# Performance work log

Measured on AMD Instinct MI355X. Metric: run time of the kernel, lower is better.

The kernel has to match this reference:

```python
import jax, jax.numpy as jnp
import numpy as np

TEMPERATURE = 0.07
N_CLASSES = 100


def setup_inputs() -> dict:
    key = jax.random.key(0)
    k1, k2 = jax.random.split(key)
    N, D = 8192, 128
    emb = jax.random.normal(k1, (N, D), dtype=jnp.float32)
    # unit-normalize so exp(sim / temperature) stays finite in fp32
    emb = emb / jnp.linalg.norm(emb, axis=1, keepdims=True)
    labels = jax.random.randint(k2, (N,), 0, N_CLASSES, dtype=jnp.int64)
    return {"embeddings": emb, "labels": labels}


def reference(embeddings, labels):
    N = embeddings.shape[0]
    dt = embeddings.dtype
    # [N, N] similarity
    sim = jnp.matmul(embeddings, embeddings.T) / TEMPERATURE
    off_diag = 1.0 - jnp.eye(N, dtype=dt)
    pos_mask = (labels[:, None] == labels[None, :]).astype(dt) * off_diag
    exp_sim = jnp.exp(sim) * off_diag  # diagonal zeroed
    positive_sum = jnp.sum(exp_sim * pos_mask, axis=1)
    total_sum = jnp.sum(exp_sim, axis=1)
    loss = -jnp.log(positive_sum / (total_sum + 1e-8) + 1e-8)
    valid = pos_mask.sum(axis=1) > 0
    cnt = jnp.sum(valid.astype(dt))
    mean_loss = jnp.where(
        cnt > 0,
        jnp.sum(jnp.where(valid, loss, jnp.zeros_like(loss))) / jnp.maximum(cnt, 1.0),
        jnp.asarray(0.0, dtype=dt),
    )
    return mean_loss
```

## Files before the change

### kernel.cpp

```cpp
#include <hip/hip_runtime.h>

#define N 8192
#define D 128
#define SCALE_A 20.6098592f
#define NBX 64
#define NBY 8
#define NBLK (NBX * NBY)

using short8  = __attribute__((ext_vector_type(8))) short;
using float4v = __attribute__((ext_vector_type(4))) float;

#if __has_builtin(__builtin_amdgcn_exp2f)
#define EXP2(x) __builtin_amdgcn_exp2f(x)
#else
#define EXP2(x) __expf((x) * 0.69314718f)
#endif

static __device__ inline unsigned int f2bf(float f) {
    union { float f; unsigned int u; } x;
    x.f = f;
    unsigned int u = x.u;
    return (u + 0x7FFFu + ((u >> 16) & 1u)) >> 16;
}

__global__ __launch_bounds__(256) void cl_prep(
    const float* __restrict__ emb, unsigned short* __restrict__ bfBf,
    unsigned short* __restrict__ bfAf, float* __restrict__ tot,
    int* __restrict__ ticket)
{
    const int t = blockIdx.x * 256 + threadIdx.x;
    const int row   = t >> 4;
    const int chunk = t & 15;
    const float* p = emb + (size_t)row * D + chunk * 8;
    float4v f0 = *(const float4v*)p;
    float4v f1 = *(const float4v*)(p + 4);
    uint4 ub, ua;
    ub.x = f2bf(f0[0]) | (f2bf(f0[1]) << 16);
    ub.y = f2bf(f0[2]) | (f2bf(f0[3]) << 16);
    ub.z = f2bf(f1[0]) | (f2bf(f1[1]) << 16);
    ub.w = f2bf(f1[2]) | (f2bf(f1[3]) << 16);
    ua.x = f2bf(f0[0] * SCALE_A) | (f2bf(f0[1] * SCALE_A) << 16);
    ua.y = f2bf(f0[2] * SCALE_A) | (f2bf(f0[3] * SCALE_A) << 16);
    ua.z = f2bf(f1[0] * SCALE_A) | (f2bf(f1[1] * SCALE_A) << 16);
    ua.w = f2bf(f1[2] * SCALE_A) | (f2bf(f1[3] * SCALE_A) << 16);
    const int rt = row >> 4, m = row & 15;
    const int ks = chunk >> 2, qq = chunk & 3;
    const int o  = ((rt * 4 + ks) << 6) + qq * 16 + m;
    ((uint4*)bfBf)[o] = ub;
    ((uint4*)bfAf)[o] = ua;
    if (t < 2 * N) tot[t] = 0.f;
    if (t == 0) *ticket = 0;
}

__global__ __launch_bounds__(256, 2) void cl_main(
    const unsigned short* __restrict__ bfAf, const unsigned short* __restrict__ bfBf,
    const int* __restrict__ labels,
    float* __restrict__ tot, float* __restrict__ pos,
    int* __restrict__ ticket, float* __restrict__ out)
{
    __shared__ float sred[2][4];
    __shared__ int s_ticket;

    const int tid  = threadIdx.x;
    const int lane = tid & 63;
    const int wave = tid >> 6;
    const int q    = lane >> 4;
    const int c    = lane & 15;
    const int rw   = blockIdx.x * 128 + wave * 32;

    const short8* Af = (const short8*)bfAf;
    const short8* Bf = (const short8*)bfBf;

    short8 afrag[2][4];
    int rowlab[2][4];
    #pragma unroll
    for (int tr = 0; tr < 2; ++tr) {
        const int rt = blockIdx.x * 8 + wave * 2 + tr;
        #pragma unroll
        for (int ks = 0; ks < 4; ++ks)
            afrag[tr][ks] = Af[((rt * 4 + ks) << 6) + lane];
        #pragma unroll
        for (int reg = 0; reg < 4; ++reg)
            rowlab[tr][reg] = labels[rw + tr * 16 + q * 4 + reg];
    }

    float tot_a[2][4] = {{0.f,0.f,0.f,0.f},{0.f,0.f,0.f,0.f}};
    float pos_a[2][4] = {{0.f,0.f,0.f,0.f},{0.f,0.f,0.f,0.f}};

    for (int it = 0; it < 8; ++it) {
        const int cbase = blockIdx.y * 1024 + it * 128;
        const int ct0   = cbase >> 4;

        int collab[8];
        #pragma unroll
        for (int tc = 0; tc < 8; ++tc) collab[tc] = labels[cbase + tc * 16 + c];

        float4v acc[2][8];
        #pragma unroll
        for (int tr = 0; tr < 2; ++tr)
            #pragma unroll
            for (int tc = 0; tc < 8; ++tc) {
                float4v z = {0.f, 0.f, 0.f, 0.f};
                acc[tr][tc] = z;
            }

        #pragma unroll
        for (int ks = 0; ks < 4; ++ks) {
            #pragma unroll
            for (int tc = 0; tc < 8; ++tc) {
                short8 b = Bf[(((ct0 + tc) * 4 + ks) << 6) + lane];
                #pragma unroll
                for (int tr = 0; tr < 2; ++tr)
                    acc[tr][tc] = __builtin_amdgcn_mfma_f32_16x16x32_bf16(
                        afrag[tr][ks], b, acc[tr][tc], 0, 0, 0);
            }
        }

        #pragma unroll
        for (int tr = 0; tr < 2; ++tr) {
            const int rtile = rw + tr * 16;
            #pragma unroll
            for (int tc = 0; tc < 8; ++tc) {
                const bool diag_tile = (rtile == cbase + tc * 16);
                const int lc = collab[tc];
                #pragma unroll
                for (int reg = 0; reg < 4; ++reg) {
                    float v = EXP2(acc[tr][tc][reg]);
                    if (diag_tile && (q * 4 + reg) == c) v = 0.f;
                    tot_a[tr][reg] += v;
                    if (rowlab[tr][reg] == lc) pos_a[tr][reg] += v;
                }
            }
        }
    }

    #pragma unroll
    for (int tr = 0; tr < 2; ++tr)
        #pragma unroll
        for (int reg = 0; reg < 4; ++reg) {
            float tt = tot_a[tr][reg];
            float pp = pos_a[tr][reg];
            #pragma unroll
            for (int m = 1; m < 16; m <<= 1) {
                tt += __shfl_xor(tt, m, 64);
                pp += __shfl_xor(pp, m, 64);
            }
            if (c == 0) {
                const int r = rw + tr * 16 + q * 4 + reg;
                atomicAdd(&tot[r], tt);
                atomicAdd(&pos[r], pp);
            }
        }

    asm volatile("s_waitcnt vmcnt(0)" ::: "memory");
    __syncthreads();
    if (tid == 0)
        s_ticket = __hip_atomic_fetch_add(ticket, 1, __ATOMIC_RELAXED,
                                          __HIP_MEMORY_SCOPE_AGENT);
    __syncthreads();
    if (s_ticket != NBLK - 1) return;

    float lsum = 0.f, lcnt = 0.f;
    #pragma unroll 4
    for (int i = tid; i < N; i += 256) {
        const float tt = __hip_atomic_load(&tot[i], __ATOMIC_RELAXED,
                                           __HIP_MEMORY_SCOPE_AGENT);
        const float pp = __hip_atomic_load(&pos[i], __ATOMIC_RELAXED,
                                           __HIP_MEMORY_SCOPE_AGENT);
        const float loss = -__logf(pp / (tt + 1e-8f) + 1e-8f);
        if (pp > 0.f) { lsum += loss; lcnt += 1.f; }
    }
    #pragma unroll
    for (int m = 1; m < 64; m <<= 1) {
        lsum += __shfl_xor(lsum, m, 64);
        lcnt += __shfl_xor(lcnt, m, 64);
    }
    if (lane == 0) { sred[0][wave] = lsum; sred[1][wave] = lcnt; }
    __syncthreads();
    if (tid == 0) {
        const float s = sred[0][0] + sred[0][1] + sred[0][2] + sred[0][3];
        const float n = sred[1][0] + sred[1][1] + sred[1][2] + sred[1][3];
        out[0] = (n > 0.f) ? s / fmaxf(n, 1.f) : 0.f;
    }
}

extern "C" void kernel_launch(void* const* d_in, const int* in_sizes, int n_in,
                              void* d_out, int out_size, void* d_ws, size_t ws_size,
                              hipStream_t stream) {
    const float* emb  = (const float*)d_in[0];
    const int* labels = (const int*)d_in[1];
    unsigned short* bfBf = (unsigned short*)d_ws;
    unsigned short* bfAf = bfBf + (size_t)N * D;
    float* tot    = (float*)(bfAf + (size_t)N * D);
    float* pos    = tot + N;
    int*   ticket = (int*)(pos + N);

    cl_prep<<<512, 256, 0, stream>>>(emb, bfBf, bfAf, tot, ticket);
    cl_main<<<dim3(NBX, NBY), 256, 0, stream>>>(bfAf, bfBf, labels, tot, pos,
                                                ticket, (float*)d_out);
}
```

Baseline: 107.2 us.

## Subtract precomputed diagonal exp term instead of masking inside the main loop

Result: slower. 112.0 us (+4.4%).

```diff
diff --git a/kernel.cpp b/kernel.cpp
--- a/kernel.cpp
+++ b/kernel.cpp
@@ -22,11 +22,16 @@
     unsigned int u = x.u;
     return (u + 0x7FFFu + ((u >> 16) & 1u)) >> 16;
 }
+static __device__ inline float bfround(float f) {
+    union { unsigned int u; float f; } x;
+    x.u = f2bf(f) << 16;
+    return x.f;
+}
 
 __global__ __launch_bounds__(256) void cl_prep(
     const float* __restrict__ emb, unsigned short* __restrict__ bfBf,
-    unsigned short* __restrict__ bfAf, float* __restrict__ tot,
-    int* __restrict__ ticket)
+    unsigned short* __restrict__ bfAf, float* __restrict__ diagv,
+    float* __restrict__ tot, int* __restrict__ ticket)
 {
     const int t = blockIdx.x * 256 + threadIdx.x;
     const int row   = t >> 4;
@@ -48,13 +53,24 @@
     const int o  = ((rt * 4 + ks) << 6) + qq * 16 + m;
     ((uint4*)bfBf)[o] = ub;
     ((uint4*)bfAf)[o] = ua;
+
+    float part = 0.f;
+    #pragma unroll
+    for (int j = 0; j < 4; ++j) {
+        part += bfround(f0[j] * SCALE_A) * bfround(f0[j]);
+        part += bfround(f1[j] * SCALE_A) * bfround(f1[j]);
+    }
+    #pragma unroll
+    for (int s = 1; s < 16; s <<= 1) part += __shfl_xor(part, s, 64);
+    if (chunk == 0) diagv[row] = part;
+
     if (t < 2 * N) tot[t] = 0.f;
     if (t == 0) *ticket = 0;
 }
 
-__global__ __launch_bounds__(256, 2) void cl_main(
+__global__ __launch_bounds__(256, 3) void cl_main(
     const unsigned short* __restrict__ bfAf, const unsigned short* __restrict__ bfBf,
-    const int* __restrict__ labels,
+    const int* __restrict__ labels, const float* __restrict__ diagv,
     float* __restrict__ tot, float* __restrict__ pos,
     int* __restrict__ ticket, float* __restrict__ out)
 {
@@ -117,21 +133,17 @@
         }
 
         #pragma unroll
-        for (int tr = 0; tr < 2; ++tr) {
-            const int rtile = rw + tr * 16;
+        for (int tr = 0; tr < 2; ++tr)
             #pragma unroll
             for (int tc = 0; tc < 8; ++tc) {
-                const bool diag_tile = (rtile == cbase + tc * 16);
                 const int lc = collab[tc];
                 #pragma unroll
                 for (int reg = 0; reg < 4; ++reg) {
                     float v = EXP2(acc[tr][tc][reg]);
-                    if (diag_tile && (q * 4 + reg) == c) v = 0.f;
                     tot_a[tr][reg] += v;
                     if (rowlab[tr][reg] == lc) pos_a[tr][reg] += v;
                 }
             }
-        }
     }
 
     #pragma unroll
@@ -163,10 +175,11 @@
     float lsum = 0.f, lcnt = 0.f;
     #pragma unroll 4
     for (int i = tid; i < N; i += 256) {
+        const float vd = EXP2(diagv[i]);
         const float tt = __hip_atomic_load(&tot[i], __ATOMIC_RELAXED,
-                                           __HIP_MEMORY_SCOPE_AGENT);
+                                           __HIP_MEMORY_SCOPE_AGENT) - vd;
         const float pp = __hip_atomic_load(&pos[i], __ATOMIC_RELAXED,
-                                           __HIP_MEMORY_SCOPE_AGENT);
+                                           __HIP_MEMORY_SCOPE_AGENT) - vd;
         const float loss = -__logf(pp / (tt + 1e-8f) + 1e-8f);
         if (pp > 0.f) { lsum += loss; lcnt += 1.f; }
     }
@@ -193,9 +206,10 @@
     unsigned short* bfAf = bfBf + (size_t)N * D;
     float* tot    = (float*)(bfAf + (size_t)N * D);
     float* pos    = tot + N;
-    int*   ticket = (int*)(pos + N);
-
-    cl_prep<<<512, 256, 0, stream>>>(emb, bfBf, bfAf, tot, ticket);
-    cl_main<<<dim3(NBX, NBY), 256, 0, stream>>>(bfAf, bfBf, labels, tot, pos,
-                                                ticket, (float*)d_out);
-}
+    float* diagv  = pos + N;
+    int*   ticket = (int*)(diagv + N);
+
+    cl_prep<<<512, 256, 0, stream>>>(emb, bfBf, bfAf, diagv, tot, ticket);
+    cl_main<<<dim3(NBX, NBY), 256, 0, stream>>>(bfAf, bfBf, labels, diagv,
+                                                tot, pos, ticket, (float*)d_out);
+}
```
